# Optimization experiments

Hardware: AMD Instinct MI355X
Metric: run time of the kernel (lower is better)

The kernel has to match this reference:

```python
import jax, jax.numpy as jnp
import numpy as np

B = 8192          # batch
D = 256           # feature_dim
H = 64            # num attention heads
HD = D // H       # head_dim = 4
NC, NB, NF, NT = 2048, 2048, 512, 768
NCLS = 26
EPS = 1e-5


def _linear_params(k, out_d, in_d):
    s = 1.0 / np.sqrt(in_d)
    kw, kb = jax.random.split(k)
    W = jax.random.uniform(kw, (out_d, in_d), minval=-s, maxval=s, dtype=jnp.float32)
    b = jax.random.uniform(kb, (out_d,), minval=-s, maxval=s, dtype=jnp.float32)
    return W, b


def setup_inputs() -> dict:
    key = jax.random.key(0)
    ks = jax.random.split(key, 16)
    inp = {
        'x_context': jax.random.normal(ks[0], (B, NC), dtype=jnp.float32),
        'x_body':    jax.random.normal(ks[1], (B, NB), dtype=jnp.float32),
        'x_face':    jax.random.normal(ks[2], (B, NF), dtype=jnp.float32),
        'x_text':    jax.random.normal(ks[3], (B, NT), dtype=jnp.float32),
    }
    inp['Wc'], inp['bc'] = _linear_params(ks[4], D, NC)
    inp['Wb'], inp['bb'] = _linear_params(ks[5], D, NB)
    inp['Wf'], inp['bf'] = _linear_params(ks[6], D, NF)
    inp['Wt'], inp['bt'] = _linear_params(ks[7], D, NT)
    # MultiheadAttention packed in-proj (3D x D) and out-proj
    inp['in_w'], inp['in_b'] = _linear_params(ks[8], 3 * D, D)
    inp['out_w'], inp['out_b'] = _linear_params(ks[9], D, D)
    # gate MLP
    inp['Wg1'], inp['bg1'] = _linear_params(ks[10], D, D)
    inp['Wg2'], inp['bg2'] = _linear_params(ks[11], 1, D)
    # fusion head
    inp['W1'], inp['b1'] = _linear_params(ks[12], D, 4 * D)
    inp['gamma'] = jnp.ones((D,), dtype=jnp.float32)
    inp['beta'] = jnp.zeros((D,), dtype=jnp.float32)
    inp['W2'], inp['b2'] = _linear_params(ks[13], NCLS, D)
    return inp


def reference(x_context, x_body, x_face, x_text,
              Wc, bc, Wb, bb, Wf, bf, Wt, bt,
              in_w, in_b, out_w, out_b,
              Wg1, bg1, Wg2, bg2,
              W1, b1, gamma, beta, W2, b2):
    # per-modality projections -> [B, 4, D]
    f = jnp.stack([
        x_context @ Wc.T + bc,
        x_body    @ Wb.T + bb,
        x_face    @ Wf.T + bf,
        x_text    @ Wt.T + bt,
    ], axis=1)
    bsz = f.shape[0]

    # MultiheadAttention with seq_len=1 per token: softmax over a single key
    Wq, Wk, Wv = jnp.split(in_w, 3, axis=0)
    bq, bk, bv = jnp.split(in_b, 3)
    q = (f @ Wq.T + bq).reshape(bsz, 4, H, HD)
    k = (f @ Wk.T + bk).reshape(bsz, 4, H, HD)
    v = (f @ Wv.T + bv).reshape(bsz, 4, H, HD)
    scores = jnp.sum(q * k, axis=-1, keepdims=True) / np.sqrt(HD)  # [B,4,H,1]
    w = jax.nn.softmax(scores, axis=-1)                            # == 1 (single key)
    attn = (w * v).reshape(bsz, 4, D)
    self_out = attn @ out_w.T + out_b                              # [B,4,D]

    # cross attention: with seq_len=1 the output depends only on key/value,
    # so each (query i, key 3-j) call equals the self-style output of modality 3-j;
    # combining over the 4 key variants reduces to the mean over modalities.
    cross = jnp.mean(self_out, axis=1, keepdims=True)              # [B,1,D]

    gate = jax.nn.sigmoid(jax.nn.relu(self_out @ Wg1.T + bg1) @ Wg2.T + bg2)  # [B,4,1]
    combined = gate * self_out + (1.0 - gate) * cross              # [B,4,D]

    h = combined.reshape(bsz, 4 * D) @ W1.T + b1                   # [B,D]
    # BatchNorm1d (training-mode batch statistics, biased variance)
    mu = jnp.mean(h, axis=0)
    var = jnp.var(h, axis=0)
    h = (h - mu) / jnp.sqrt(var + EPS) * gamma + beta
    h = jax.nn.relu(h)                                             # dropout = identity (eval)
    return h @ W2.T + b2                                           # [B,26]
```

## Files before the change

### kernel.cpp

```cpp
#include <hip/hip_runtime.h>
#include <math.h>

typedef __attribute__((ext_vector_type(8))) short bf16x8;
typedef __attribute__((ext_vector_type(4))) short bf16x4;
typedef __attribute__((ext_vector_type(4))) float f32x4;
typedef unsigned short u16;
typedef unsigned int u32;

#define BSZ   8192
#define BN_EPS 1e-5f

__device__ inline u16 f2bf(float x) {
    u32 u = __float_as_uint(x);
    u32 r = (u + 0x7FFFu + ((u >> 16) & 1u)) >> 16;
    return (u16)r;
}
__device__ inline float bf2f_lo(u32 p) { return __uint_as_float(p << 16); }
__device__ inline float bf2f_hi(u32 p) { return __uint_as_float(p & 0xFFFF0000u); }

__device__ inline void async_g2l(const void* g, void* l) {
    __builtin_amdgcn_global_load_lds(
        (const __attribute__((address_space(1))) void*)g,
        (__attribute__((address_space(3))) void*)l, 16, 0, 0);
}

__global__ __launch_bounds__(256)
void wvo_kernel(const float* __restrict__ in_w, const float* __restrict__ in_b,
                const float* __restrict__ out_w, const float* __restrict__ out_b,
                float* __restrict__ wvo, float* __restrict__ bvo)
{
    const int i = blockIdx.x;
    const int j = threadIdx.x;
    const float* Wv = in_w + 512 * 256;
    float s = 0.f;
#pragma unroll 8
    for (int k = 0; k < 256; ++k)
        s = fmaf(out_w[i * 256 + k], Wv[k * 256 + j], s);
    wvo[i * 256 + j] = s;
    if (i == 0) {
        const float* bv = in_b + 512;
        float t = 0.f;
        for (int k = 0; k < 256; ++k)
            t = fmaf(out_w[j * 256 + k], bv[k], t);
        bvo[j] = t + out_b[j];
    }
}

__global__ __launch_bounds__(256)
void cvt_weights(const float* __restrict__ wvo, const float* __restrict__ Wc,
                 const float* __restrict__ Wb,  const float* __restrict__ Wf,
                 const float* __restrict__ Wt,  const float* __restrict__ Wg1,
                 const float* __restrict__ W1f, u16* __restrict__ dst)
{
    int gid = blockIdx.x * 256 + threadIdx.x;
    const float* src; u16* d; int loc;
    if      (gid <   8192) { src = wvo; d = dst + 0;       loc = gid; }
    else if (gid <  73728) { src = Wc;  d = dst + 65536;   loc = gid - 8192; }
    else if (gid < 139264) { src = Wb;  d = dst + 589824;  loc = gid - 73728; }
    else if (gid < 155648) { src = Wf;  d = dst + 1114112; loc = gid - 139264; }
    else if (gid < 180224) { src = Wt;  d = dst + 1245184; loc = gid - 155648; }
    else if (gid < 188416) { src = Wg1; d = dst + 1441792; loc = gid - 180224; }
    else                   { src = W1f; d = dst + 1507328; loc = gid - 188416; }
    const float4 v0 = *(const float4*)(src + (size_t)loc * 8);
    const float4 v1 = *(const float4*)(src + (size_t)loc * 8 + 4);
    uint4 o;
    o.x = (u32)f2bf(v0.x) | ((u32)f2bf(v0.y) << 16);
    o.y = (u32)f2bf(v0.z) | ((u32)f2bf(v0.w) << 16);
    o.z = (u32)f2bf(v1.x) | ((u32)f2bf(v1.y) << 16);
    o.w = (u32)f2bf(v1.z) | ((u32)f2bf(v1.w) << 16);
    *(uint4*)(d + (size_t)loc * 8) = o;
}

__global__ __launch_bounds__(256)
void gemm_proj(const float* __restrict__ A0, const float* __restrict__ A1,
               const float* __restrict__ A2, const float* __restrict__ A3,
               const u16* __restrict__ Wp0, const u16* __restrict__ Wp1,
               const u16* __restrict__ Wp2, const u16* __restrict__ Wp3,
               const float* __restrict__ b0, const float* __restrict__ b1,
               const float* __restrict__ b2, const float* __restrict__ b3,
               u16* __restrict__ fb)
{
    __shared__ u16 As[2][1024];
    __shared__ u16 Bs[2][8192];
    const int m = blockIdx.y;
    const float* A  = (m == 0) ? A0 : (m == 1) ? A1 : (m == 2) ? A2 : A3;
    const u16* Wp   = (m == 0) ? Wp0 : (m == 1) ? Wp1 : (m == 2) ? Wp2 : Wp3;
    const float* bi = (m == 0) ? b0 : (m == 1) ? b1 : (m == 2) ? b2 : b3;
    const int K     = (m == 0) ? 2048 : (m == 1) ? 2048 : (m == 2) ? 512 : 768;
    const int nt = K >> 5;

    const int t = threadIdx.x;
    const int w = t >> 6, l = t & 63;
    const int bm = blockIdx.x * 32;
    const int arow = t >> 3, ac4 = (t & 7) * 4;

    float4 ar;
    auto loadA = [&](int k0) {
        ar = *(const float4*)(A + (size_t)(bm + arow) * K + k0 + ac4);
    };
    auto writeA = [&](int buf) {
        bf16x4 p;
        p[0] = (short)f2bf(ar.x); p[1] = (short)f2bf(ar.y);
        p[2] = (short)f2bf(ar.z); p[3] = (short)f2bf(ar.w);
        *(bf16x4*)((char*)As[buf] + arow * 64 + (t & 7) * 8) = p;
    };
    auto issueB = [&](int k0, int buf) {
#pragma unroll
        for (int it = 0; it < 4; ++it) {
            const int n0 = (w * 4 + it) * 16;
            async_g2l(Wp + (size_t)(n0 + (l >> 2)) * K + k0 + (l & 3) * 8,
                      Bs[buf] + n0 * 32);
        }
    };

    f32x4 acc[2][4];
    const f32x4 z = {0.f, 0.f, 0.f, 0.f};
#pragma unroll
    for (int i = 0; i < 2; ++i)
#pragma unroll
        for (int j = 0; j < 4; ++j) acc[i][j] = z;

    loadA(0);
    issueB(0, 0);
    writeA(0);
    __syncthreads();

    for (int t0 = 0; t0 < nt; ++t0) {
        const int cur = t0 & 1;
        if (t0 + 1 < nt) { loadA((t0 + 1) * 32); issueB((t0 + 1) * 32, cur ^ 1); }
        const char* ab = (const char*)As[cur];
        const char* bb = (const char*)Bs[cur];
        bf16x8 af[2], bq[4];
#pragma unroll
        for (int i = 0; i < 2; ++i)
            af[i] = *(const bf16x8*)(ab + (i * 16 + (l & 15)) * 64 + (l >> 4) * 16);
#pragma unroll
        for (int j = 0; j < 4; ++j)
            bq[j] = *(const bf16x8*)(bb + (w * 64 + j * 16 + (l & 15)) * 64 + (l >> 4) * 16);
#pragma unroll
        for (int i = 0; i < 2; ++i)
#pragma unroll
            for (int j = 0; j < 4; ++j)
                acc[i][j] = __builtin_amdgcn_mfma_f32_16x16x32_bf16(
                    af[i], bq[j], acc[i][j], 0, 0, 0);
        if (t0 + 1 < nt) writeA(cur ^ 1);
        __syncthreads();
    }

#pragma unroll
    for (int j = 0; j < 4; ++j) {
        const int col = w * 64 + j * 16 + (l & 15);
        const float bv = bi[col];
#pragma unroll
        for (int i = 0; i < 2; ++i)
#pragma unroll
            for (int r = 0; r < 4; ++r) {
                const int rt = i * 16 + ((l >> 4) << 2) + r;
                fb[((size_t)(bm + rt) * 4 + m) * 256 + col] = f2bf(acc[i][j][r] + bv);
            }
    }
}

__global__ __launch_bounds__(256)
void fused_sgc(const u16* __restrict__ fb, const u16* __restrict__ wvo_bf,
               const float* __restrict__ bvo,
               const u16* __restrict__ wg1_bf, const float* __restrict__ bg1,
               const float* __restrict__ wg2, const float* __restrict__ bg2,
               u16* __restrict__ comb)
{
    __shared__ u16 FS[8192];
    __shared__ u16 Bs[2][8192];
    __shared__ float gp[4][32];
    __shared__ float gate_s[32];
    const int t = threadIdx.x, w = t >> 6, l = t & 63;
    const int bm = blockIdx.x * 32;
    char* const fs = (char*)FS;

#pragma unroll
    for (int it = 0; it < 4; ++it) {
        const int r0 = (w * 4 + it) * 2;
        const int row = r0 + (l >> 5);
        const int ch = (l & 31) ^ (row & 7);
        async_g2l(fb + (size_t)(bm + row) * 256 + ch * 8, FS + r0 * 256);
    }
    auto issueB = [&](const u16* Wp, int k0, int buf) {
#pragma unroll
        for (int it = 0; it < 4; ++it) {
            const int n0 = (w * 4 + it) * 16;
            async_g2l(Wp + (size_t)(n0 + (l >> 2)) * 256 + k0 + (l & 3) * 8,
                      Bs[buf] + n0 * 32);
        }
    };
    issueB(wvo_bf, 0, 0);
    __syncthreads();

    const f32x4 z = {0.f, 0.f, 0.f, 0.f};

    f32x4 acc[2][4];
#pragma unroll
    for (int i = 0; i < 2; ++i)
#pragma unroll
        for (int j = 0; j < 4; ++j) acc[i][j] = z;

    for (int ks = 0; ks < 8; ++ks) {
        const int cur = ks & 1;
        if (ks < 7) issueB(wvo_bf, (ks + 1) * 32, cur ^ 1);
        else        issueB(wg1_bf, 0, 0);
        bf16x8 af[2], bq[4];
#pragma unroll
        for (int i = 0; i < 2; ++i) {
            const int row = i * 16 + (l & 15);
            af[i] = *(const bf16x8*)(fs + row * 512 +
                      (((ks * 4 + (l >> 4)) ^ (row & 7)) << 4));
        }
#pragma unroll
        for (int j = 0; j < 4; ++j)
            bq[j] = *(const bf16x8*)((char*)Bs[cur] +
                      (w * 64 + j * 16 + (l & 15)) * 64 + (l >> 4) * 16);
#pragma unroll
        for (int i = 0; i < 2; ++i)
#pragma unroll
            for (int j = 0; j < 4; ++j)
                acc[i][j] = __builtin_amdgcn_mfma_f32_16x16x32_bf16(
                    af[i], bq[j], acc[i][j], 0, 0, 0);
        __syncthreads();
    }

#pragma unroll
    for (int j = 0; j < 4; ++j) {
        const int col = w * 64 + j * 16 + (l & 15);
        const float bv = bvo[col];
#pragma unroll
        for (int i = 0; i < 2; ++i)
#pragma unroll
            for (int r = 0; r < 4; ++r) {
                const int rt = i * 16 + ((l >> 4) << 2) + r;
                *(u16*)(fs + rt * 512 + (((col >> 3) ^ (rt & 7)) << 4) + (col & 7) * 2)
                    = f2bf(acc[i][j][r] + bv);
            }
    }
    __syncthreads();

    f32x4 g2[2][4];
#pragma unroll
    for (int i = 0; i < 2; ++i)
#pragma unroll
        for (int j = 0; j < 4; ++j) g2[i][j] = z;

    for (int ks = 0; ks < 8; ++ks) {
        const int cur = ks & 1;
        if (ks < 7) issueB(wg1_bf, (ks + 1) * 32, cur ^ 1);
        bf16x8 af[2], bq[4];
#pragma unroll
        for (int i = 0; i < 2; ++i) {
            const int row = i * 16 + (l & 15);
            af[i] = *(const bf16x8*)(fs + row * 512 +
                      (((ks * 4 + (l >> 4)) ^ (row & 7)) << 4));
        }
#pragma unroll
        for (int j = 0; j < 4; ++j)
            bq[j] = *(const bf16x8*)((char*)Bs[cur] +
                      (w * 64 + j * 16 + (l & 15)) * 64 + (l >> 4) * 16);
#pragma unroll
        for (int i = 0; i < 2; ++i)
#pragma unroll
            for (int j = 0; j < 4; ++j)
                g2[i][j] = __builtin_amdgcn_mfma_f32_16x16x32_bf16(
                    af[i], bq[j], g2[i][j], 0, 0, 0);
        __syncthreads();
    }

    {
        float s[2][4];
#pragma unroll
        for (int i = 0; i < 2; ++i)
#pragma unroll
            for (int r = 0; r < 4; ++r) s[i][r] = 0.f;
#pragma unroll
        for (int j = 0; j < 4; ++j) {
            const int col = w * 64 + j * 16 + (l & 15);
            const float bv = bg1[col], wv = wg2[col];
#pragma unroll
            for (int i = 0; i < 2; ++i)
#pragma unroll
                for (int r = 0; r < 4; ++r)
                    s[i][r] += fmaxf(g2[i][j][r] + bv, 0.f) * wv;
        }
#pragma unroll
        for (int off = 1; off < 16; off <<= 1)
#pragma unroll
            for (int i = 0; i < 2; ++i)
#pragma unroll
                for (int r = 0; r < 4; ++r)
                    s[i][r] += __shfl_xor(s[i][r], off);
        if ((l & 15) == 0) {
#pragma unroll
            for (int i = 0; i < 2; ++i)
#pragma unroll
                for (int r = 0; r < 4; ++r)
                    gp[w][i * 16 + ((l >> 4) << 2) + r] = s[i][r];
        }
    }
    __syncthreads();
    if (t < 32) {
        const float g = gp[0][t] + gp[1][t] + gp[2][t] + gp[3][t] + bg2[0];
        gate_s[t] = 1.f / (1.f + expf(-g));
    }
    __syncthreads();

    u32* const comb32 = (u32*)comb;
    const int p2 = t & 127;
    const int gh = t >> 7;
#pragma unroll
    for (int gg = 0; gg < 4; ++gg) {
        const int g = gh * 4 + gg;
        const int d0 = p2 * 2;
        float lo4[4], hi4[4], gv[4];
#pragma unroll
        for (int mm = 0; mm < 4; ++mm) {
            const int row = g * 4 + mm;
            const u32 v = *(const u32*)(fs + row * 512 +
                            (((d0 >> 3) ^ (row & 7)) << 4) + (d0 & 7) * 2);
            lo4[mm] = bf2f_lo(v); hi4[mm] = bf2f_hi(v);
            gv[mm] = gate_s[g * 4 + mm];
        }
        const float cl = 0.25f * (lo4[0] + lo4[1] + lo4[2] + lo4[3]);
        const float ch = 0.25f * (hi4[0] + hi4[1] + hi4[2] + hi4[3]);
#pragma unroll
        for (int mm = 0; mm < 4; ++mm) {
            const float ol = gv[mm] * lo4[mm] + (1.f - gv[mm]) * cl;
            const float oh = gv[mm] * hi4[mm] + (1.f - gv[mm]) * ch;
            comb32[(size_t)(bm + g * 4 + mm) * 128 + p2] =
                (u32)f2bf(ol) | ((u32)f2bf(oh) << 16);
        }
    }
}

__global__ __launch_bounds__(256)
void gemm_w1(const u16* __restrict__ combp, const u16* __restrict__ w1p,
             const float* __restrict__ b1p, float* __restrict__ h)
{
    __shared__ u16 As[2][1024];
    __shared__ u16 Bs[2][8192];
    const int t = threadIdx.x, w = t >> 6, l = t & 63;
    const int bm = blockIdx.x * 32;
    const int nt = 32;

    auto issueA = [&](int k0, int buf) {
        if (w < 2) {
            const int r0 = w * 16;
            async_g2l(combp + (size_t)(bm + r0 + (l >> 2)) * 1024 + k0 + (l & 3) * 8,
                      As[buf] + r0 * 32);
        }
    };
    auto issueB = [&](int k0, int buf) {
#pragma unroll
        for (int it = 0; it < 4; ++it) {
            const int n0 = (w * 4 + it) * 16;
            async_g2l(w1p + (size_t)(n0 + (l >> 2)) * 1024 + k0 + (l & 3) * 8,
                      Bs[buf] + n0 * 32);
        }
    };

    f32x4 acc[2][4];
    const f32x4 z = {0.f, 0.f, 0.f, 0.f};
#pragma unroll
    for (int i = 0; i < 2; ++i)
#pragma unroll
        for (int j = 0; j < 4; ++j) acc[i][j] = z;

    issueA(0, 0);
    issueB(0, 0);
    __syncthreads();

    for (int t0 = 0; t0 < nt; ++t0) {
        const int cur = t0 & 1;
        if (t0 + 1 < nt) { issueA((t0 + 1) * 32, cur ^ 1); issueB((t0 + 1) * 32, cur ^ 1); }
        const char* ab = (const char*)As[cur];
        const char* bb = (const char*)Bs[cur];
        bf16x8 af[2], bq[4];
#pragma unroll
        for (int i = 0; i < 2; ++i)
            af[i] = *(const bf16x8*)(ab + (i * 16 + (l & 15)) * 64 + (l >> 4) * 16);
#pragma unroll
        for (int j = 0; j < 4; ++j)
            bq[j] = *(const bf16x8*)(bb + (w * 64 + j * 16 + (l & 15)) * 64 + (l >> 4) * 16);
#pragma unroll
        for (int i = 0; i < 2; ++i)
#pragma unroll
            for (int j = 0; j < 4; ++j)
                acc[i][j] = __builtin_amdgcn_mfma_f32_16x16x32_bf16(
                    af[i], bq[j], acc[i][j], 0, 0, 0);
        __syncthreads();
    }

#pragma unroll
    for (int j = 0; j < 4; ++j) {
        const int col = w * 64 + j * 16 + (l & 15);
        const float bv = b1p[col];
#pragma unroll
        for (int i = 0; i < 2; ++i)
#pragma unroll
            for (int r = 0; r < 4; ++r) {
                const int rt = i * 16 + ((l >> 4) << 2) + r;
                h[(size_t)(bm + rt) * 256 + col] = acc[i][j][r] + bv;
            }
    }
}

__global__ __launch_bounds__(256)
void bn_part(const float* __restrict__ h, float* __restrict__ psum,
             float* __restrict__ psq)
{
    const int p = blockIdx.x;
    const int d = threadIdx.x;
    float s = 0.f, q = 0.f;
#pragma unroll 8
    for (int r = 0; r < 32; ++r) {
        const float v = h[((size_t)p * 32 + r) * 256 + d];
        s += v;
        q = fmaf(v, v, q);
    }
    psum[p * 256 + d] = s;
    psq[p * 256 + d]  = q;
}

__global__ __launch_bounds__(256)
void bn_fin(const float* __restrict__ psum, const float* __restrict__ psq,
            const float* __restrict__ gamma, const float* __restrict__ beta,
            float* __restrict__ scale, float* __restrict__ shift)
{
    const int d = threadIdx.x;
    float s = 0.f, q = 0.f;
#pragma unroll 8
    for (int p = 0; p < 256; ++p) { s += psum[p * 256 + d]; q += psq[p * 256 + d]; }
    const float mu  = s * (1.f / BSZ);
    const float var = q * (1.f / BSZ) - mu * mu;
    const float inv = rsqrtf(var + BN_EPS);
    const float sc  = gamma[d] * inv;
    scale[d] = sc;
    shift[d] = beta[d] - mu * sc;
}

__global__ __launch_bounds__(256)
void final_kernel(const float* __restrict__ h, const float* __restrict__ scale,
                  const float* __restrict__ shift, const float* __restrict__ W2,
                  const float* __restrict__ b2, float* __restrict__ out)
{
    __shared__ float W2s[26][260];
    __shared__ float scs[256], shs[256];
    const int t = threadIdx.x;
    for (int u = t; u < 26 * 256; u += 256) {
        const int c = u >> 8, n = u & 255;
        W2s[c][(n >> 6) * 65 + (n & 63)] = W2[u];
    }
    scs[t] = scale[t];
    shs[t] = shift[t];
    __syncthreads();

    const int r = blockIdx.x * 64 + (t >> 2);
    const int p = t & 3;
    float acc[26];
#pragma unroll
    for (int c = 0; c < 26; ++c) acc[c] = 0.f;
    const float* hr = h + (size_t)r * 256 + p * 64;
#pragma unroll
    for (int i4 = 0; i4 < 16; ++i4) {
        const float4 v4 = *(const float4*)(hr + i4 * 4);
#pragma unroll
        for (int q = 0; q < 4; ++q) {
            const int i = i4 * 4 + q;
            const int n = p * 64 + i;
            const float vv = (q == 0) ? v4.x : (q == 1) ? v4.y : (q == 2) ? v4.z : v4.w;
            const float v = fmaxf(fmaf(vv, scs[n], shs[n]), 0.f);
            const int sw = p * 65 + i;
#pragma unroll
            for (int c = 0; c < 26; ++c)
                acc[c] = fmaf(v, W2s[c][sw], acc[c]);
        }
    }
#pragma unroll
    for (int off = 1; off < 4; off <<= 1)
#pragma unroll
        for (int c = 0; c < 26; ++c)
            acc[c] += __shfl_xor(acc[c], off);
    if (p == 0) {
#pragma unroll
        for (int c = 0; c < 26; ++c)
            out[(size_t)r * 26 + c] = acc[c] + b2[c];
    }
}

extern "C" void kernel_launch(void* const* d_in, const int* in_sizes, int n_in,
                              void* d_out, int out_size, void* d_ws, size_t ws_size,
                              hipStream_t stream)
{
    const float* x_ctx  = (const float*)d_in[0];
    const float* x_body = (const float*)d_in[1];
    const float* x_face = (const float*)d_in[2];
    const float* x_text = (const float*)d_in[3];
    const float* Wc = (const float*)d_in[4];  const float* bc = (const float*)d_in[5];
    const float* Wb = (const float*)d_in[6];  const float* bb = (const float*)d_in[7];
    const float* Wf = (const float*)d_in[8];  const float* bf = (const float*)d_in[9];
    const float* Wt = (const float*)d_in[10]; const float* bt = (const float*)d_in[11];
    const float* in_w  = (const float*)d_in[12]; const float* in_b  = (const float*)d_in[13];
    const float* out_w = (const float*)d_in[14]; const float* out_b = (const float*)d_in[15];
    const float* Wg1 = (const float*)d_in[16]; const float* bg1 = (const float*)d_in[17];
    const float* Wg2 = (const float*)d_in[18]; const float* bg2 = (const float*)d_in[19];
    const float* W1  = (const float*)d_in[20]; const float* b1  = (const float*)d_in[21];
    const float* gamma = (const float*)d_in[22]; const float* beta = (const float*)d_in[23];
    const float* W2  = (const float*)d_in[24]; const float* b2  = (const float*)d_in[25];

    char* wsb = (char*)d_ws;
    u16*   f_bf  = (u16*)(wsb + 0);
    u16*   comb  = f_bf;
    float* h     = (float*)(wsb + (16u << 20));
    u16*   wpb   = (u16*)(wsb + (32u << 20));
    float* wvo   = (float*)(wsb + (36u << 20));
    float* bvo   = (float*)(wsb + (36u << 20) + 262144);
    float* psum  = (float*)(wsb + (37u << 20));
    float* psq   = (float*)(wsb + (37u << 20) + 262144);
    float* scale = (float*)(wsb + (37u << 20) + 524288);
    float* shift = (float*)(wsb + (37u << 20) + 528384);

    u16* wvo_bf = wpb + 0;
    u16* wc_bf  = wpb + 65536;
    u16* wb_bf  = wpb + 589824;
    u16* wf_bf  = wpb + 1114112;
    u16* wt_bf  = wpb + 1245184;
    u16* wg1_bf = wpb + 1441792;
    u16* w1_bf  = wpb + 1507328;

    wvo_kernel<<<256, 256, 0, stream>>>(in_w, in_b, out_w, out_b, wvo, bvo);
    cvt_weights<<<864, 256, 0, stream>>>(wvo, Wc, Wb, Wf, Wt, Wg1, W1, wpb);

    gemm_proj<<<dim3(256, 4), 256, 0, stream>>>(x_ctx, x_body, x_face, x_text,
                                                wc_bf, wb_bf, wf_bf, wt_bf,
                                                bc, bb, bf, bt, f_bf);

    fused_sgc<<<1024, 256, 0, stream>>>(f_bf, wvo_bf, bvo, wg1_bf, bg1,
                                        Wg2, bg2, comb);

    gemm_w1<<<256, 256, 0, stream>>>(comb, w1_bf, b1, h);

    bn_part<<<256, 256, 0, stream>>>(h, psum, psq);
    bn_fin<<<1, 256, 0, stream>>>(psum, psq, gamma, beta, scale, shift);
    final_kernel<<<128, 256, 0, stream>>>(h, scale, shift, W2, b2, (float*)d_out);
}
```

Baseline: 170.0 us.

## Enlarge projection GEMM tiles, swizzle LDS, and deepen load pipeline

```diff
diff --git a/kernel.cpp b/kernel.cpp
--- a/kernel.cpp
+++ b/kernel.cpp
@@ -80,71 +80,122 @@
                const float* __restrict__ b2, const float* __restrict__ b3,
                u16* __restrict__ fb)
 {
-    __shared__ u16 As[2][1024];
-    __shared__ u16 Bs[2][8192];
+    __shared__ u16 As[2][4096];
+    __shared__ u16 Bs[2][16384];
     const int m = blockIdx.y;
     const float* A  = (m == 0) ? A0 : (m == 1) ? A1 : (m == 2) ? A2 : A3;
     const u16* Wp   = (m == 0) ? Wp0 : (m == 1) ? Wp1 : (m == 2) ? Wp2 : Wp3;
     const float* bi = (m == 0) ? b0 : (m == 1) ? b1 : (m == 2) ? b2 : b3;
     const int K     = (m == 0) ? 2048 : (m == 1) ? 2048 : (m == 2) ? 512 : 768;
-    const int nt = K >> 5;
+    const int nt = K >> 6;
 
     const int t = threadIdx.x;
     const int w = t >> 6, l = t & 63;
-    const int bm = blockIdx.x * 32;
-    const int arow = t >> 3, ac4 = (t & 7) * 4;
-
-    float4 ar;
-    auto loadA = [&](int k0) {
-        ar = *(const float4*)(A + (size_t)(bm + arow) * K + k0 + ac4);
+    const int bm = blockIdx.x * 64;
+    const int arow = t >> 2, akq = t & 3;
+
+    float4 rA[4], rB[4];
+    auto loadA = [&](int k0, float4* r) {
+        const float* g = A + (size_t)(bm + arow) * K + k0 + akq * 16;
+#pragma unroll
+        for (int q = 0; q < 4; ++q) r[q] = *(const float4*)(g + q * 4);
     };
-    auto writeA = [&](int buf) {
-        bf16x4 p;
-        p[0] = (short)f2bf(ar.x); p[1] = (short)f2bf(ar.y);
-        p[2] = (short)f2bf(ar.z); p[3] = (short)f2bf(ar.w);
-        *(bf16x4*)((char*)As[buf] + arow * 64 + (t & 7) * 8) = p;
+    auto writeA = [&](int buf, const float4* r) {
+        bf16x8 p0, p1;
+        p0[0] = (short)f2bf(r[0].x); p0[1] = (short)f2bf(r[0].y);
+        p0[2] = (short)f2bf(r[0].z); p0[3] = (short)f2bf(r[0].w);
+        p0[4] = (short)f2bf(r[1].x); p0[5] = (short)f2bf(r[1].y);
+        p0[6] = (short)f2bf(r[1].z); p0[7] = (short)f2bf(r[1].w);
+        p1[0] = (short)f2bf(r[2].x); p1[1] = (short)f2bf(r[2].y);
+        p1[2] = (short)f2bf(r[2].z); p1[3] = (short)f2bf(r[2].w);
+        p1[4] = (short)f2bf(r[3].x); p1[5] = (short)f2bf(r[3].y);
+        p1[6] = (short)f2bf(r[3].z); p1[7] = (short)f2bf(r[3].w);
+        char* abw = (char*)As[buf];
+        *(bf16x8*)(abw + arow * 128 + (((akq * 2 + 0) ^ (arow & 7)) << 4)) = p0;
+        *(bf16x8*)(abw + arow * 128 + (((akq * 2 + 1) ^ (arow & 7)) << 4)) = p1;
     };
     auto issueB = [&](int k0, int buf) {
 #pragma unroll
-        for (int it = 0; it < 4; ++it) {
-            const int n0 = (w * 4 + it) * 16;
-            async_g2l(Wp + (size_t)(n0 + (l >> 2)) * K + k0 + (l & 3) * 8,
-                      Bs[buf] + n0 * 32);
+        for (int it = 0; it < 8; ++it) {
+            const int n  = it * 32 + w * 8 + (l >> 3);
+            const int ch = (l & 7) ^ (n & 7);
+            async_g2l(Wp + (size_t)n * K + k0 + ch * 8, Bs[buf] + it * 2048 + w * 512);
         }
     };
 
-    f32x4 acc[2][4];
+    f32x4 acc[4][4];
     const f32x4 z = {0.f, 0.f, 0.f, 0.f};
 #pragma unroll
-    for (int i = 0; i < 2; ++i)
+    for (int i = 0; i < 4; ++i)
 #pragma unroll
         for (int j = 0; j < 4; ++j) acc[i][j] = z;
 
-    loadA(0);
+    auto compute = [&](const char* abr, const char* bbr) {
+#pragma unroll
+        for (int kk = 0; kk < 2; ++kk) {
+            bf16x8 af[4], bq[4];
+            const int ch = kk * 4 + (l >> 4);
+#pragma unroll
+            for (int i = 0; i < 4; ++i) {
+                const int fr = i * 16 + (l & 15);
+                af[i] = *(const bf16x8*)(abr + fr * 128 + ((ch ^ (fr & 7)) << 4));
+            }
+#pragma unroll
+            for (int j = 0; j < 4; ++j) {
+                const int n = w * 64 + j * 16 + (l & 15);
+                bq[j] = *(const bf16x8*)(bbr + n * 128 + ((ch ^ (n & 7)) << 4));
+            }
+#pragma unroll
+            for (int i = 0; i < 4; ++i)
+#pragma unroll
+                for (int j = 0; j < 4; ++j)
+                    acc[i][j] = __builtin_amdgcn_mfma_f32_16x16x32_bf16(
+                        af[i], bq[j], acc[i][j], 0, 0, 0);
+        }
+    };
+
+    loadA(0, rA);
+    writeA(0, rA);
     issueB(0, 0);
-    writeA(0);
-    __syncthreads();
-
-    for (int t0 = 0; t0 < nt; ++t0) {
-        const int cur = t0 & 1;
-        if (t0 + 1 < nt) { loadA((t0 + 1) * 32); issueB((t0 + 1) * 32, cur ^ 1); }
-        const char* ab = (const char*)As[cur];
-        const char* bb = (const char*)Bs[cur];
-        bf16x8 af[2], bq[4];
-#pragma unroll
-        for (int i = 0; i < 2; ++i)
-            af[i] = *(const bf16x8*)(ab + (i * 16 + (l & 15)) * 64 + (l >> 4) * 16);
-#pragma unroll
-        for (int j = 0; j < 4; ++j)
-            bq[j] = *(const bf16x8*)(bb + (w * 64 + j * 16 + (l & 15)) * 64 + (l >> 4) * 16);
-#pragma unroll
-        for (int i = 0; i < 2; ++i)
-#pragma unroll
-            for (int j = 0; j < 4; ++j)
-                acc[i][j] = __builtin_amdgcn_mfma_f32_16x16x32_bf16(
-                    af[i], bq[j], acc[i][j], 0, 0, 0);
-        if (t0 + 1 < nt) writeA(cur ^ 1);
-        __syncthreads();
+    loadA(64, rB);
+    issueB(64, 1);
+    loadA(128, rA);
+    asm volatile("s_waitcnt vmcnt(16) lgkmcnt(0)" ::: "memory");
+    __builtin_amdgcn_sched_barrier(0);
+    __builtin_amdgcn_s_barrier();
+
+    for (int t0 = 0; t0 < nt; t0 += 2) {
+        compute((const char*)As[0], (const char*)Bs[0]);
+        writeA(1, rB);
+        __builtin_amdgcn_s_barrier();
+        if (t0 + 3 < nt) {
+            loadA((t0 + 3) * 64, rB);
+            issueB((t0 + 2) * 64, 0);
+            asm volatile("s_waitcnt vmcnt(12) lgkmcnt(0)" ::: "memory");
+        } else if (t0 + 2 < nt) {
+            issueB((t0 + 2) * 64, 0);
+            asm volatile("s_waitcnt vmcnt(8) lgkmcnt(0)" ::: "memory");
+        } else {
+            asm volatile("s_waitcnt vmcnt(0) lgkmcnt(0)" ::: "memory");
+        }
+        __builtin_amdgcn_sched_barrier(0);
+        __builtin_amdgcn_s_barrier();
+
+        compute((const char*)As[1], (const char*)Bs[1]);
+        if (t0 + 2 < nt) writeA(0, rA);
+        __builtin_amdgcn_s_barrier();
+        if (t0 + 4 < nt) {
+            loadA((t0 + 4) * 64, rA);
+            issueB((t0 + 3) * 64, 1);
+            asm volatile("s_waitcnt vmcnt(12) lgkmcnt(0)" ::: "memory");
+        } else if (t0 + 3 < nt) {
+            issueB((t0 + 3) * 64, 1);
+            asm volatile("s_waitcnt vmcnt(8) lgkmcnt(0)" ::: "memory");
+        } else {
+            asm volatile("s_waitcnt vmcnt(0) lgkmcnt(0)" ::: "memory");
+        }
+        __builtin_amdgcn_sched_barrier(0);
+        __builtin_amdgcn_s_barrier();
     }
 
 #pragma unroll
@@ -152,7 +203,7 @@
         const int col = w * 64 + j * 16 + (l & 15);
         const float bv = bi[col];
 #pragma unroll
-        for (int i = 0; i < 2; ++i)
+        for (int i = 0; i < 4; ++i)
 #pragma unroll
             for (int r = 0; r < 4; ++r) {
                 const int rt = i * 16 + ((l >> 4) << 2) + r;
@@ -534,7 +585,7 @@
     wvo_kernel<<<256, 256, 0, stream>>>(in_w, in_b, out_w, out_b, wvo, bvo);
     cvt_weights<<<864, 256, 0, stream>>>(wvo, Wc, Wb, Wf, Wt, Wg1, W1, wpb);
 
-    gemm_proj<<<dim3(256, 4), 256, 0, stream>>>(x_ctx, x_body, x_face, x_text,
+    gemm_proj<<<dim3(128, 4), 256, 0, stream>>>(x_ctx, x_body, x_face, x_text,
                                                 wc_bf, wb_bf, wf_bf, wt_bf,
                                                 bc, bb, bf, bt, f_bf);
 
```

After: 153.9 us. 1.1x faster.

## Fold value/out-projection into modality weights and retile projection GEMM to 128x128

Applied to the files above, without the earlier changes.

```diff
diff --git a/kernel.cpp b/kernel.cpp
--- a/kernel.cpp
+++ b/kernel.cpp
@@ -2,7 +2,6 @@
 #include <math.h>
 
 typedef __attribute__((ext_vector_type(8))) short bf16x8;
-typedef __attribute__((ext_vector_type(4))) short bf16x4;
 typedef __attribute__((ext_vector_type(4))) float f32x4;
 typedef unsigned short u16;
 typedef unsigned int u32;
@@ -47,20 +46,66 @@
 }
 
 __global__ __launch_bounds__(256)
-void cvt_weights(const float* __restrict__ wvo, const float* __restrict__ Wc,
-                 const float* __restrict__ Wb,  const float* __restrict__ Wf,
-                 const float* __restrict__ Wt,  const float* __restrict__ Wg1,
+void wfold(const float* __restrict__ wvo, const float* __restrict__ bvo,
+           const float* __restrict__ Wc, const float* __restrict__ Wb,
+           const float* __restrict__ Wf, const float* __restrict__ Wt,
+           const float* __restrict__ bc, const float* __restrict__ bb,
+           const float* __restrict__ bfc, const float* __restrict__ btx,
+           float* __restrict__ wff, float* __restrict__ bfold)
+{
+    const int bx = blockIdx.x;
+    const int t = threadIdx.x;
+    if (bx == 168) {
+        if (t < 256) {
+#pragma unroll
+            for (int m = 0; m < 4; ++m) {
+                const float* bm = (m == 0) ? bc : (m == 1) ? bb : (m == 2) ? bfc : btx;
+                float s = 0.f;
+                for (int j = 0; j < 256; ++j)
+                    s = fmaf(wvo[t * 256 + j], bm[j], s);
+                bfold[m * 256 + t] = s + bvo[t];
+            }
+        }
+        return;
+    }
+    const float* W; float* out; int K, c0;
+    if      (bx <  64) { W = Wc; out = wff + 0;       K = 2048; c0 = bx * 32; }
+    else if (bx < 128) { W = Wb; out = wff + 524288;  K = 2048; c0 = (bx - 64) * 32; }
+    else if (bx < 144) { W = Wf; out = wff + 1048576; K = 512;  c0 = (bx - 128) * 32; }
+    else               { W = Wt; out = wff + 1179648; K = 768;  c0 = (bx - 144) * 32; }
+
+    __shared__ float ws[256][32];
+#pragma unroll
+    for (int q = 0; q < 8; ++q) {
+        const float4 v = *(const float4*)(W + (size_t)t * K + c0 + q * 4);
+        ws[t][q * 4 + 0] = v.x; ws[t][q * 4 + 1] = v.y;
+        ws[t][q * 4 + 2] = v.z; ws[t][q * 4 + 3] = v.w;
+    }
+    __syncthreads();
+
+    float acc[32];
+#pragma unroll
+    for (int c = 0; c < 32; ++c) acc[c] = 0.f;
+    for (int j = 0; j < 256; ++j) {
+        const float wv = wvo[t * 256 + j];
+#pragma unroll
+        for (int c = 0; c < 32; ++c)
+            acc[c] = fmaf(wv, ws[j][c], acc[c]);
+    }
+#pragma unroll
+    for (int c = 0; c < 32; ++c)
+        out[(size_t)t * K + c0 + c] = acc[c];
+}
+
+__global__ __launch_bounds__(256)
+void cvt_weights(const float* __restrict__ wff, const float* __restrict__ Wg1,
                  const float* __restrict__ W1f, u16* __restrict__ dst)
 {
     int gid = blockIdx.x * 256 + threadIdx.x;
     const float* src; u16* d; int loc;
-    if      (gid <   8192) { src = wvo; d = dst + 0;       loc = gid; }
-    else if (gid <  73728) { src = Wc;  d = dst + 65536;   loc = gid - 8192; }
-    else if (gid < 139264) { src = Wb;  d = dst + 589824;  loc = gid - 73728; }
-    else if (gid < 155648) { src = Wf;  d = dst + 1114112; loc = gid - 139264; }
-    else if (gid < 180224) { src = Wt;  d = dst + 1245184; loc = gid - 155648; }
-    else if (gid < 188416) { src = Wg1; d = dst + 1441792; loc = gid - 180224; }
-    else                   { src = W1f; d = dst + 1507328; loc = gid - 188416; }
+    if      (gid < 172032) { src = wff; d = dst + 0;       loc = gid; }
+    else if (gid < 180224) { src = Wg1; d = dst + 1376256; loc = gid - 172032; }
+    else                   { src = W1f; d = dst + 1441792; loc = gid - 180224; }
     const float4 v0 = *(const float4*)(src + (size_t)loc * 8);
     const float4 v1 = *(const float4*)(src + (size_t)loc * 8 + 4);
     uint4 o;
@@ -72,51 +117,70 @@
 }
 
 __global__ __launch_bounds__(256)
-void gemm_proj(const float* __restrict__ A0, const float* __restrict__ A1,
-               const float* __restrict__ A2, const float* __restrict__ A3,
-               const u16* __restrict__ Wp0, const u16* __restrict__ Wp1,
-               const u16* __restrict__ Wp2, const u16* __restrict__ Wp3,
-               const float* __restrict__ b0, const float* __restrict__ b1,
-               const float* __restrict__ b2, const float* __restrict__ b3,
-               u16* __restrict__ fb)
-{
-    __shared__ u16 As[2][1024];
+void gemm_so(const float* __restrict__ x0, const float* __restrict__ x1,
+             const float* __restrict__ x2, const float* __restrict__ x3,
+             const u16* __restrict__ wpb, const float* __restrict__ bfold,
+             u16* __restrict__ so)
+{
+    __shared__ u16 As[2][8192];
     __shared__ u16 Bs[2][8192];
-    const int m = blockIdx.y;
-    const float* A  = (m == 0) ? A0 : (m == 1) ? A1 : (m == 2) ? A2 : A3;
-    const u16* Wp   = (m == 0) ? Wp0 : (m == 1) ? Wp1 : (m == 2) ? Wp2 : Wp3;
-    const float* bi = (m == 0) ? b0 : (m == 1) ? b1 : (m == 2) ? b2 : b3;
-    const int K     = (m == 0) ? 2048 : (m == 1) ? 2048 : (m == 2) ? 512 : 768;
-    const int nt = K >> 5;
+    const int m  = blockIdx.z;
+    const int by = blockIdx.y;
+    const float* A = (m == 0) ? x0 : (m == 1) ? x1 : (m == 2) ? x2 : x3;
+    const int K    = (m == 0) ? 2048 : (m == 1) ? 2048 : (m == 2) ? 512 : 768;
+    const u16* Wp  = wpb + ((m == 0) ? 0 : (m == 1) ? 524288 :
+                            (m == 2) ? 1048576 : 1179648) + (size_t)by * 128 * K;
+    const float* bias = bfold + m * 256 + by * 128;
+    const int nt = K >> 6;
 
     const int t = threadIdx.x;
     const int w = t >> 6, l = t & 63;
-    const int bm = blockIdx.x * 32;
-    const int arow = t >> 3, ac4 = (t & 7) * 4;
-
-    float4 ar;
+    const int wr = w >> 1, wc = w & 1;
+    const int bm = blockIdx.x * 128;
+    const int arow = t >> 2, akq = t & 3;
+
+    float4 rA[8];
     auto loadA = [&](int k0) {
-        ar = *(const float4*)(A + (size_t)(bm + arow) * K + k0 + ac4);
+        const float* g0 = A + (size_t)(bm + arow) * K + k0 + akq * 16;
+        const float* g1 = g0 + (size_t)64 * K;
+#pragma unroll
+        for (int q = 0; q < 4; ++q) {
+            rA[q]     = *(const float4*)(g0 + q * 4);
+            rA[4 + q] = *(const float4*)(g1 + q * 4);
+        }
     };
     auto writeA = [&](int buf) {
-        bf16x4 p;
-        p[0] = (short)f2bf(ar.x); p[1] = (short)f2bf(ar.y);
-        p[2] = (short)f2bf(ar.z); p[3] = (short)f2bf(ar.w);
-        *(bf16x4*)((char*)As[buf] + arow * 64 + (t & 7) * 8) = p;
+        char* ab = (char*)As[buf];
+#pragma unroll
+        for (int half = 0; half < 2; ++half) {
+            const int r = arow + half * 64;
+            const float4* rr = rA + half * 4;
+            bf16x8 p0, p1;
+            p0[0] = (short)f2bf(rr[0].x); p0[1] = (short)f2bf(rr[0].y);
+            p0[2] = (short)f2bf(rr[0].z); p0[3] = (short)f2bf(rr[0].w);
+            p0[4] = (short)f2bf(rr[1].x); p0[5] = (short)f2bf(rr[1].y);
+            p0[6] = (short)f2bf(rr[1].z); p0[7] = (short)f2bf(rr[1].w);
+            p1[0] = (short)f2bf(rr[2].x); p1[1] = (short)f2bf(rr[2].y);
+            p1[2] = (short)f2bf(rr[2].z); p1[3] = (short)f2bf(rr[2].w);
+            p1[4] = (short)f2bf(rr[3].x); p1[5] = (short)f2bf(rr[3].y);
+            p1[6] = (short)f2bf(rr[3].z); p1[7] = (short)f2bf(rr[3].w);
+            *(bf16x8*)(ab + r * 128 + (((akq * 2 + 0) ^ (r & 7)) << 4)) = p0;
+            *(bf16x8*)(ab + r * 128 + (((akq * 2 + 1) ^ (r & 7)) << 4)) = p1;
+        }
     };
     auto issueB = [&](int k0, int buf) {
 #pragma unroll
         for (int it = 0; it < 4; ++it) {
-            const int n0 = (w * 4 + it) * 16;
-            async_g2l(Wp + (size_t)(n0 + (l >> 2)) * K + k0 + (l & 3) * 8,
-                      Bs[buf] + n0 * 32);
+            const int n  = it * 32 + w * 8 + (l >> 3);
+            const int ch = (l & 7) ^ (n & 7);
+            async_g2l(Wp + (size_t)n * K + k0 + ch * 8, Bs[buf] + it * 2048 + w * 512);
         }
     };
 
-    f32x4 acc[2][4];
+    f32x4 acc[4][4];
     const f32x4 z = {0.f, 0.f, 0.f, 0.f};
 #pragma unroll
-    for (int i = 0; i < 2; ++i)
+    for (int i = 0; i < 4; ++i)
 #pragma unroll
         for (int j = 0; j < 4; ++j) acc[i][j] = z;
 
@@ -127,46 +191,53 @@
 
     for (int t0 = 0; t0 < nt; ++t0) {
         const int cur = t0 & 1;
-        if (t0 + 1 < nt) { loadA((t0 + 1) * 32); issueB((t0 + 1) * 32, cur ^ 1); }
-        const char* ab = (const char*)As[cur];
-        const char* bb = (const char*)Bs[cur];
-        bf16x8 af[2], bq[4];
-#pragma unroll
-        for (int i = 0; i < 2; ++i)
-            af[i] = *(const bf16x8*)(ab + (i * 16 + (l & 15)) * 64 + (l >> 4) * 16);
-#pragma unroll
-        for (int j = 0; j < 4; ++j)
-            bq[j] = *(const bf16x8*)(bb + (w * 64 + j * 16 + (l & 15)) * 64 + (l >> 4) * 16);
-#pragma unroll
-        for (int i = 0; i < 2; ++i)
-#pragma unroll
-            for (int j = 0; j < 4; ++j)
-                acc[i][j] = __builtin_amdgcn_mfma_f32_16x16x32_bf16(
-                    af[i], bq[j], acc[i][j], 0, 0, 0);
+        if (t0 + 1 < nt) { loadA((t0 + 1) * 64); issueB((t0 + 1) * 64, cur ^ 1); }
+        const char* abr = (const char*)As[cur];
+        const char* bbr = (const char*)Bs[cur];
+#pragma unroll
+        for (int kk = 0; kk < 2; ++kk) {
+            bf16x8 af[4], bq[4];
+            const int ch = kk * 4 + (l >> 4);
+#pragma unroll
+            for (int i = 0; i < 4; ++i) {
+                const int fr = wr * 64 + i * 16 + (l & 15);
+                af[i] = *(const bf16x8*)(abr + fr * 128 + ((ch ^ (fr & 7)) << 4));
+            }
+#pragma unroll
+            for (int j = 0; j < 4; ++j) {
+                const int n = wc * 64 + j * 16 + (l & 15);
+                bq[j] = *(const bf16x8*)(bbr + n * 128 + ((ch ^ (n & 7)) << 4));
+            }
+#pragma unroll
+            for (int i = 0; i < 4; ++i)
+#pragma unroll
+                for (int j = 0; j < 4; ++j)
+                    acc[i][j] = __builtin_amdgcn_mfma_f32_16x16x32_bf16(
+                        af[i], bq[j], acc[i][j], 0, 0, 0);
+        }
         if (t0 + 1 < nt) writeA(cur ^ 1);
         __syncthreads();
     }
 
 #pragma unroll
     for (int j = 0; j < 4; ++j) {
-        const int col = w * 64 + j * 16 + (l & 15);
-        const float bv = bi[col];
-#pragma unroll
-        for (int i = 0; i < 2; ++i)
+        const int cl = wc * 64 + j * 16 + (l & 15);
+        const int col = by * 128 + cl;
+        const float bv = bias[cl];
+#pragma unroll
+        for (int i = 0; i < 4; ++i)
 #pragma unroll
             for (int r = 0; r < 4; ++r) {
-                const int rt = i * 16 + ((l >> 4) << 2) + r;
-                fb[((size_t)(bm + rt) * 4 + m) * 256 + col] = f2bf(acc[i][j][r] + bv);
+                const int rl = wr * 64 + i * 16 + ((l >> 4) << 2) + r;
+                so[((size_t)(bm + rl) * 4 + m) * 256 + col] = f2bf(acc[i][j][r] + bv);
             }
     }
 }
 
 __global__ __launch_bounds__(256)
-void fused_sgc(const u16* __restrict__ fb, const u16* __restrict__ wvo_bf,
-               const float* __restrict__ bvo,
-               const u16* __restrict__ wg1_bf, const float* __restrict__ bg1,
-               const float* __restrict__ wg2, const float* __restrict__ bg2,
-               u16* __restrict__ comb)
+void fused_gc(const u16* __restrict__ so, const u16* __restrict__ wg1_bf,
+              const float* __restrict__ bg1, const float* __restrict__ wg2,
+              const float* __restrict__ bg2, u16* __restrict__ comb)
 {
     __shared__ u16 FS[8192];
     __shared__ u16 Bs[2][8192];
@@ -181,75 +252,29 @@
         const int r0 = (w * 4 + it) * 2;
         const int row = r0 + (l >> 5);
         const int ch = (l & 31) ^ (row & 7);
-        async_g2l(fb + (size_t)(bm + row) * 256 + ch * 8, FS + r0 * 256);
-    }
-    auto issueB = [&](const u16* Wp, int k0, int buf) {
+        async_g2l(so + (size_t)(bm + row) * 256 + ch * 8, FS + r0 * 256);
+    }
+    auto issueB = [&](int k0, int buf) {
 #pragma unroll
         for (int it = 0; it < 4; ++it) {
             const int n0 = (w * 4 + it) * 16;
-            async_g2l(Wp + (size_t)(n0 + (l >> 2)) * 256 + k0 + (l & 3) * 8,
+            async_g2l(wg1_bf + (size_t)(n0 + (l >> 2)) * 256 + k0 + (l & 3) * 8,
                       Bs[buf] + n0 * 32);
         }
     };
-    issueB(wvo_bf, 0, 0);
+    issueB(0, 0);
     __syncthreads();
 
     const f32x4 z = {0.f, 0.f, 0.f, 0.f};
-
-    f32x4 acc[2][4];
+    f32x4 g2[2][4];
 #pragma unroll
     for (int i = 0; i < 2; ++i)
 #pragma unroll
-        for (int j = 0; j < 4; ++j) acc[i][j] = z;
+        for (int j = 0; j < 4; ++j) g2[i][j] = z;
 
     for (int ks = 0; ks < 8; ++ks) {
         const int cur = ks & 1;
-        if (ks < 7) issueB(wvo_bf, (ks + 1) * 32, cur ^ 1);
-        else        issueB(wg1_bf, 0, 0);
-        bf16x8 af[2], bq[4];
-#pragma unroll
-        for (int i = 0; i < 2; ++i) {
-            const int row = i * 16 + (l & 15);
-            af[i] = *(const bf16x8*)(fs + row * 512 +
-                      (((ks * 4 + (l >> 4)) ^ (row & 7)) << 4));
-        }
-#pragma unroll
-        for (int j = 0; j < 4; ++j)
-            bq[j] = *(const bf16x8*)((char*)Bs[cur] +
-                      (w * 64 + j * 16 + (l & 15)) * 64 + (l >> 4) * 16);
-#pragma unroll
-        for (int i = 0; i < 2; ++i)
-#pragma unroll
-            for (int j = 0; j < 4; ++j)
-                acc[i][j] = __builtin_amdgcn_mfma_f32_16x16x32_bf16(
-                    af[i], bq[j], acc[i][j], 0, 0, 0);
-        __syncthreads();
-    }
-
-#pragma unroll
-    for (int j = 0; j < 4; ++j) {
-        const int col = w * 64 + j * 16 + (l & 15);
-        const float bv = bvo[col];
-#pragma unroll
-        for (int i = 0; i < 2; ++i)
-#pragma unroll
-            for (int r = 0; r < 4; ++r) {
-                const int rt = i * 16 + ((l >> 4) << 2) + r;
-                *(u16*)(fs + rt * 512 + (((col >> 3) ^ (rt & 7)) << 4) + (col & 7) * 2)
-                    = f2bf(acc[i][j][r] + bv);
-            }
-    }
-    __syncthreads();
-
-    f32x4 g2[2][4];
-#pragma unroll
-    for (int i = 0; i < 2; ++i)
-#pragma unroll
-        for (int j = 0; j < 4; ++j) g2[i][j] = z;
-
-    for (int ks = 0; ks < 8; ++ks) {
-        const int cur = ks & 1;
-        if (ks < 7) issueB(wg1_bf, (ks + 1) * 32, cur ^ 1);
+        if (ks < 7) issueB((ks + 1) * 32, cur ^ 1);
         bf16x8 af[2], bq[4];
 #pragma unroll
         for (int i = 0; i < 2; ++i) {
@@ -512,34 +537,31 @@
     const float* W2  = (const float*)d_in[24]; const float* b2  = (const float*)d_in[25];
 
     char* wsb = (char*)d_ws;
-    u16*   f_bf  = (u16*)(wsb + 0);
-    u16*   comb  = f_bf;
+    u16*   so_bf = (u16*)(wsb + 0);
+    u16*   comb  = so_bf;
     float* h     = (float*)(wsb + (16u << 20));
-    u16*   wpb   = (u16*)(wsb + (32u << 20));
-    float* wvo   = (float*)(wsb + (36u << 20));
-    float* bvo   = (float*)(wsb + (36u << 20) + 262144);
-    float* psum  = (float*)(wsb + (37u << 20));
-    float* psq   = (float*)(wsb + (37u << 20) + 262144);
-    float* scale = (float*)(wsb + (37u << 20) + 524288);
-    float* shift = (float*)(wsb + (37u << 20) + 528384);
-
-    u16* wvo_bf = wpb + 0;
-    u16* wc_bf  = wpb + 65536;
-    u16* wb_bf  = wpb + 589824;
-    u16* wf_bf  = wpb + 1114112;
-    u16* wt_bf  = wpb + 1245184;
-    u16* wg1_bf = wpb + 1441792;
-    u16* w1_bf  = wpb + 1507328;
+    u16*   wpb   = (u16*)(wsb + (24u << 20));
+    float* wff   = (float*)(wsb + (28u << 20));
+    float* wvo   = (float*)(wsb + (34u << 20));
+    float* bvo   = (float*)(wsb + (34u << 20) + 262144);
+    float* bfold = (float*)(wsb + (34u << 20) + 266240);
+    float* psum  = (float*)(wsb + (35u << 20));
+    float* psq   = (float*)(wsb + (35u << 20) + 262144);
+    float* scale = (float*)(wsb + (35u << 20) + 524288);
+    float* shift = (float*)(wsb + (35u << 20) + 528384);
+
+    u16* wg1_bf = wpb + 1376256;
+    u16* w1_bf  = wpb + 1441792;
 
     wvo_kernel<<<256, 256, 0, stream>>>(in_w, in_b, out_w, out_b, wvo, bvo);
-    cvt_weights<<<864, 256, 0, stream>>>(wvo, Wc, Wb, Wf, Wt, Wg1, W1, wpb);
-
-    gemm_proj<<<dim3(256, 4), 256, 0, stream>>>(x_ctx, x_body, x_face, x_text,
-                                                wc_bf, wb_bf, wf_bf, wt_bf,
-                                                bc, bb, bf, bt, f_bf);
-
-    fused_sgc<<<1024, 256, 0, stream>>>(f_bf, wvo_bf, bvo, wg1_bf, bg1,
-                                        Wg2, bg2, comb);
+    wfold<<<169, 256, 0, stream>>>(wvo, bvo, Wc, Wb, Wf, Wt, bc, bb, bf, bt,
+                                   wff, bfold);
+    cvt_weights<<<832, 256, 0, stream>>>(wff, Wg1, W1, wpb);
+
+    gemm_so<<<dim3(64, 2, 4), 256, 0, stream>>>(x_ctx, x_body, x_face, x_text,
+                                                wpb, bfold, so_bf);
+
+    fused_gc<<<1024, 256, 0, stream>>>(so_bf, wg1_bf, bg1, Wg2, bg2, comb);
 
     gemm_w1<<<256, 256, 0, stream>>>(comb, w1_bf, b1, h);
 
```

New measurement: 186.0 us. 9.4% more time.
